# Kernel optimization log

Hardware: AMD Instinct MI355X
Metric: run time of the kernel (lower is better)

The kernel has to match this reference:

```python
import jax, jax.numpy as jnp
import numpy as np
from jax import lax

EPS = 1e-4


def setup_inputs() -> dict:
    key = jax.random.key(0)
    k1, k2, k3, k4, k5 = jax.random.split(key, 5)
    B, F, P, C = 8192, 512, 64, 100
    return {
        "x": jax.random.normal(k1, (B, F), dtype=jnp.float32),
        "w": jax.random.normal(k2, (P, F), dtype=jnp.float32),
        "xi": jax.random.normal(k3, (1, P), dtype=jnp.float32),
        "eta": jax.random.normal(k4, (1, P), dtype=jnp.float32),
        "beta": jax.random.normal(k5, (P, C), dtype=jnp.float32),
    }


def reference(x, w, xi, eta, beta):
    # Distance layer: squared Euclidean distance to each prototype -> [B, P]
    # ||w_p - x||^2 expressed as GEMM form (same math, efficient)
    d = (jnp.sum(x * x, axis=-1, keepdims=True)
         - 2.0 * (x @ w.T)
         + jnp.sum(w * w, axis=-1))  # [B, P]

    # Distance activation: si = sigmoid(xi) * exp(-eta^2 * d), scaled by per-sample max
    gamma = eta * eta                       # [1, P]
    alpha = jax.nn.sigmoid(xi)              # [1, P]
    si = jnp.exp(-gamma * d) * alpha        # [B, P]
    si = si / (jnp.max(si, axis=-1, keepdims=True) + EPS)

    # Belief masses: u_p normalized beta^2 rows -> mass [B, P, C]
    beta_sq = beta * beta
    u = beta_sq / jnp.sum(beta_sq, axis=-1, keepdims=True)  # [P, C]
    mass = si[..., None] * u[None]                           # [B, P, C]

    # Omega: append residual uncertainty channel -> [B, P, C+1]
    omega = 1.0 - jnp.sum(mass, axis=-1, keepdims=True)
    mass_omega = jnp.concatenate([mass, omega], axis=-1)

    # Sequential Dempster combination over prototypes
    masses = jnp.moveaxis(mass_omega, 1, 0)  # [P, B, C+1]

    def step(m1, m2):
        omega1 = m1[..., -1:]
        omega2 = m2[..., -1:]
        c = m1 * m2 + m1 * omega2 + omega1 * m2
        c = c / (jnp.sum(c, axis=-1, keepdims=True) + EPS)
        return c, None

    m_final, _ = lax.scan(step, masses[0], masses[1:])  # [B, C+1]

    # Final normalization
    return m_final / jnp.sum(m_final, axis=-1, keepdims=True)
```

## Files before the change

kernel.cpp:

```cpp
#include <hip/hip_runtime.h>
#include <math.h>

#define NB 8192
#define NF 512
#define NP 64
#define NC 100
#define NR 16
#define EPSF 1e-4f
#define LOG2E  1.44269504088896340736f

using short8  = __attribute__((ext_vector_type(8))) short;
using floatx4 = __attribute__((ext_vector_type(4))) float;

__device__ __forceinline__ unsigned pk2(float a, float b) {
  return (__float_as_uint(b) & 0xffff0000u) | (__float_as_uint(a) >> 16);
}
__device__ __forceinline__ uint2 pkbf(float4 v) {
  uint2 r; r.x = pk2(v.x, v.y); r.y = pk2(v.z, v.w); return r;
}

#define OFF_XH    0
#define OFF_WH    4352
#define OFF_U     0
#define OFF_SI    21760
#define OFF_PK4   25856
#define OFF_REDB  34048
#define OFF_RMAX  35072
#define OFF_UMAX  35328
#define OFF_XSQL  35584
#define OFF_WSQL  35648
#define OFF_KGAM  35904
#define OFF_ALPH  36160
#define OFF_OMF   36416
#define SMEM_SZ   36448

__global__ __launch_bounds__(256, 2)
void ds_one(const float* __restrict__ x, const float* __restrict__ w,
            const float* __restrict__ xi, const float* __restrict__ eta,
            const float* __restrict__ beta, float* __restrict__ out)
{
  __shared__ __align__(16) char smem[SMEM_SZ];
  short*          xh    = (short*)(smem + OFF_XH);
  short*          wh    = (short*)(smem + OFF_WH);
  unsigned short* u_l   = (unsigned short*)(smem + OFF_U);
  float*          si_l  = (float*)(smem + OFF_SI);
  float4*         pk4   = (float4*)(smem + OFF_PK4);
  float*          redb  = (float*)(smem + OFF_REDB);
  float*          rmax  = (float*)(smem + OFF_RMAX);
  float*          umaxl = (float*)(smem + OFF_UMAX);
  float*          xsql  = (float*)(smem + OFF_XSQL);
  float*          wsql  = (float*)(smem + OFF_WSQL);
  float*          kgaml = (float*)(smem + OFF_KGAM);
  float*          alphl = (float*)(smem + OFF_ALPH);
  float*          omf   = (float*)(smem + OFF_OMF);

  const int t    = threadIdx.x;
  const int R0   = blockIdx.x * NR;
  const int wv   = t >> 6;
  const int wl   = t & 63;
  const int ml   = wl & 15;
  const int qd   = wl >> 4;
  const int pcol = wv * 16 + ml;
  const int xrow = t >> 4, xq = t & 15;

  float xsq_acc = 0.f;
  float wacc[4] = {0.f, 0.f, 0.f, 0.f};
  floatx4 acc = {0.f, 0.f, 0.f, 0.f};
  float4 xr0, xr1, wr[4][2];

  {
    const float* xp = &x[(size_t)(R0 + xrow) * NF + xq * 8];
    xr0 = *(const float4*)&xp[0];  xr1 = *(const float4*)&xp[4];
    #pragma unroll
    for (int g = 0; g < 4; ++g) {
      const int row = wv * 16 + g * 4 + (wl >> 4);
      const float* wp = &w[(size_t)row * NF + xq * 8];
      wr[g][0] = *(const float4*)&wp[0];  wr[g][1] = *(const float4*)&wp[4];
    }
  }
  for (int ch = 0; ch < 4; ++ch) {
    __syncthreads();
    {
      xsq_acc += xr0.x*xr0.x + xr0.y*xr0.y + xr0.z*xr0.z + xr0.w*xr0.w
               + xr1.x*xr1.x + xr1.y*xr1.y + xr1.z*xr1.z + xr1.w*xr1.w;
      *(uint2*)&xh[xrow * 136 + xq * 8]     = pkbf(xr0);
      *(uint2*)&xh[xrow * 136 + xq * 8 + 4] = pkbf(xr1);
    }
    #pragma unroll
    for (int g = 0; g < 4; ++g) {
      const int row = wv * 16 + g * 4 + (wl >> 4);
      float4 a = wr[g][0], b = wr[g][1];
      wacc[g] += a.x*a.x + a.y*a.y + a.z*a.z + a.w*a.w
               + b.x*b.x + b.y*b.y + b.z*b.z + b.w*b.w;
      *(uint2*)&wh[row * 136 + xq * 8]     = pkbf(a);
      *(uint2*)&wh[row * 136 + xq * 8 + 4] = pkbf(b);
    }
    __syncthreads();
    if (ch < 3) {
      const int kb = (ch + 1) * 128;
      const float* xp = &x[(size_t)(R0 + xrow) * NF + kb + xq * 8];
      xr0 = *(const float4*)&xp[0];  xr1 = *(const float4*)&xp[4];
      #pragma unroll
      for (int g = 0; g < 4; ++g) {
        const int row = wv * 16 + g * 4 + (wl >> 4);
        const float* wp = &w[(size_t)row * NF + kb + xq * 8];
        wr[g][0] = *(const float4*)&wp[0];  wr[g][1] = *(const float4*)&wp[4];
      }
    }
    #pragma unroll
    for (int ks = 0; ks < 4; ++ks) {
      short8 a = *(const short8*)&xh[ml * 136 + ks * 32 + qd * 8];
      short8 b = *(const short8*)&wh[(wv * 16 + ml) * 136 + ks * 32 + qd * 8];
      acc = __builtin_amdgcn_mfma_f32_16x16x32_bf16(a, b, acc, 0, 0, 0);
    }
  }

  const int p4 = t >> 2, q4 = t & 3;
  {
    const float* br = beta + p4 * NC + q4 * 25;
    float s = 0.f;
    #pragma unroll 5
    for (int j = 0; j < 25; ++j) { float b = br[j]; s = fmaf(b, b, s); }
    redb[q4 * 64 + p4] = s;
  }
  {
    float s = xsq_acc;
    s += __shfl_xor(s, 1, 64); s += __shfl_xor(s, 2, 64);
    s += __shfl_xor(s, 4, 64); s += __shfl_xor(s, 8, 64);
    if (xq == 0) xsql[xrow] = s;
  }
  #pragma unroll
  for (int g = 0; g < 4; ++g) {
    float s = wacc[g];
    s += __shfl_xor(s, 1, 64); s += __shfl_xor(s, 2, 64);
    s += __shfl_xor(s, 4, 64); s += __shfl_xor(s, 8, 64);
    if (xq == 0) wsql[wv * 16 + g * 4 + (wl >> 4)] = s;
  }
  if (t < 64) {
    float e = eta[t];
    kgaml[t] = -LOG2E * e * e;
    alphl[t] = 1.f / (1.f + __expf(-xi[t]));
  }
  __syncthreads();

  float si4[4];
  {
    const float wq = wsql[pcol], kg = kgaml[pcol], al = alphl[pcol];
    #pragma unroll
    for (int i = 0; i < 4; ++i) {
      float d = xsql[qd * 4 + i] + wq - 2.f * acc[i];
      si4[i] = al * exp2f(kg * d);
    }
    #pragma unroll
    for (int i = 0; i < 4; ++i) {
      float m = si4[i];
      m = fmaxf(m, __shfl_xor(m, 1, 64)); m = fmaxf(m, __shfl_xor(m, 2, 64));
      m = fmaxf(m, __shfl_xor(m, 4, 64)); m = fmaxf(m, __shfl_xor(m, 8, 64));
      if (ml == 0) rmax[(qd * 4 + i) * 4 + wv] = m;
    }
  }
  __syncthreads();

  #pragma unroll
  for (int i = 0; i < 4; ++i) {
    const int row = qd * 4 + i;
    float m = fmaxf(fmaxf(rmax[row * 4 + 0], rmax[row * 4 + 1]),
                    fmaxf(rmax[row * 4 + 2], rmax[row * 4 + 3]));
    si_l[row * 64 + pcol] = si4[i] * (1.f / (m + EPSF));
  }
  {
    const float bi = 1.f / (((redb[p4] + redb[64 + p4]) + redb[128 + p4]) + redb[192 + p4]);
    float um = 0.f;
    #pragma unroll
    for (int i2 = 0; i2 < 8; ++i2) {
      const int q = q4 + 4 * i2;
      float4 uv = make_float4(0.f, 0.f, 0.f, 0.f);
      if (q < 25) {
        const float* br = beta + p4 * NC + q * 4;
        uv.x = br[0]*br[0]*bi; uv.y = br[1]*br[1]*bi;
        uv.z = br[2]*br[2]*bi; uv.w = br[3]*br[3]*bi;
      }
      um = fmaxf(um, fmaxf(fmaxf(uv.x, uv.y), fmaxf(uv.z, uv.w)));
      *(uint2*)&u_l[p4 * 128 + q * 4] = pkbf(uv);
    }
    um = fmaxf(um, __shfl_xor(um, 1, 64));
    um = fmaxf(um, __shfl_xor(um, 2, 64));
    if (q4 == 0) umaxl[p4] = um;
  }
  __syncthreads();

  const int lane = t & 31;
  const int row8 = t >> 5;
  #pragma unroll 1
  for (int pass = 0; pass < 2; ++pass) {
    const int srow = pass * 8 + row8;
    {
      float sp0 = si_l[srow * 64 + lane];
      float sp1 = si_l[srow * 64 + 32 + lane];
      float um0 = umaxl[lane], um1 = umaxl[32 + lane];
      float om0 = 1.f - sp0, om1 = 1.f - sp1;
      float c0 = 1.f / fmaf(sp0, um0, om0);
      float c1 = 1.f / fmaf(sp1, um1, om1);
      float st0 = sp0 * c0, ot0 = om0 * c0;
      float st1 = sp1 * c1, ot1 = om1 * c1;
      float pA = 3.f * ot0, pB = 3.f * ot1;
      #pragma unroll
      for (int d2 = 1; d2 < 32; d2 <<= 1) {
        float uA = __shfl_up(pA, d2, 32);
        float uB = __shfl_up(pB, d2, 32);
        if (lane >= d2) { pA *= uA; pB *= uB; }
      }
      float totA = __shfl(pA, 31, 32);
      float w0 = (lane == 0) ? 0.f : pA * (1.f / 9.f);
      float w1 = (totA * pB) * (1.f / 9.f);
      pk4[row8 * 64 + lane]      = make_float4(st0, ot0, w0, 0.f);
      pk4[row8 * 64 + 32 + lane] = make_float4(st1, ot1, w1, 0.f);
      if (lane == 31) omf[row8] = (totA * pB) * (1.f / 3.f);
    }
    float4 T = make_float4(1.f, 1.f, 1.f, 1.f);
    float4 S = make_float4(0.f, 0.f, 0.f, 0.f);
    for (int p = 63; p >= 0; --p) {
      float4 f  = pk4[row8 * 64 + p];
      uint2 ud  = *(const uint2*)&u_l[p * 128 + lane * 4];
      float u0 = __uint_as_float(ud.x << 16);
      float u1 = __uint_as_float(ud.x & 0xffff0000u);
      float u2 = __uint_as_float(ud.y << 16);
      float u3 = __uint_as_float(ud.y & 0xffff0000u);
      S.x = fmaf(f.z, T.x, S.x); S.y = fmaf(f.z, T.y, S.y);
      S.z = fmaf(f.z, T.z, S.z); S.w = fmaf(f.z, T.w, S.w);
      T.x *= fmaf(f.x, u0, f.y);
      T.y *= fmaf(f.x, u1, f.y);
      T.z *= fmaf(f.x, u2, f.y);
      T.w *= fmaf(f.x, u3, f.y);
    }
    float om = omf[row8];
    float m0 = fmaf(2.f, S.x, T.x) - om;
    float m1 = fmaf(2.f, S.y, T.y) - om;
    float m2 = fmaf(2.f, S.z, T.z) - om;
    float m3 = fmaf(2.f, S.w, T.w) - om;
    if (lane >= 25) { m0 = 0.f; m1 = 0.f; m2 = 0.f; m3 = 0.f; }
    float ss = (m0 + m1) + (m2 + m3);
    #pragma unroll
    for (int msk = 1; msk < 32; msk <<= 1) ss += __shfl_xor(ss, msk, 32);
    float rn = 1.f / (ss + om);
    float* orow = &out[(size_t)(R0 + srow) * 101];
    if (lane < 25) {
      orow[lane * 4 + 0] = m0 * rn; orow[lane * 4 + 1] = m1 * rn;
      orow[lane * 4 + 2] = m2 * rn; orow[lane * 4 + 3] = m3 * rn;
    } else if (lane == 25) {
      orow[100] = om * rn;
    }
  }
}

extern "C" void kernel_launch(void* const* d_in, const int* in_sizes, int n_in,
                              void* d_out, int out_size, void* d_ws, size_t ws_size,
                              hipStream_t stream)
{
  const float* x    = (const float*)d_in[0];
  const float* w    = (const float*)d_in[1];
  const float* xi   = (const float*)d_in[2];
  const float* eta  = (const float*)d_in[3];
  const float* beta = (const float*)d_in[4];
  (void)d_ws; (void)ws_size;
  hipLaunchKernelGGL(ds_one, dim3(NB / NR), dim3(256), 0, stream,
                     x, w, xi, eta, beta, (float*)d_out);
}
```

Baseline: 84.54 us.

## Split Dempster prototype chain across wave halves with register-cached masses

Result: no change. 84.50 us (-0.1%).

```diff
diff --git a/kernel.cpp b/kernel.cpp
--- a/kernel.cpp
+++ b/kernel.cpp
@@ -18,21 +18,23 @@
 __device__ __forceinline__ uint2 pkbf(float4 v) {
   uint2 r; r.x = pk2(v.x, v.y); r.y = pk2(v.z, v.w); return r;
 }
+__device__ __forceinline__ float rlane(float v, int l) {
+  return __uint_as_float(__builtin_amdgcn_readlane(__float_as_uint(v), l));
+}
 
 #define OFF_XH    0
 #define OFF_WH    4352
 #define OFF_U     0
 #define OFF_SI    21760
 #define OFF_PK4   25856
-#define OFF_REDB  34048
-#define OFF_RMAX  35072
-#define OFF_UMAX  35328
-#define OFF_XSQL  35584
-#define OFF_WSQL  35648
-#define OFF_KGAM  35904
-#define OFF_ALPH  36160
-#define OFF_OMF   36416
-#define SMEM_SZ   36448
+#define OFF_REDB  29952
+#define OFF_RMAX  30976
+#define OFF_UMAX  31232
+#define OFF_XSQL  31488
+#define OFF_WSQL  31552
+#define OFF_KGAM  31808
+#define OFF_ALPH  32064
+#define SMEM_SZ   32320
 
 __global__ __launch_bounds__(256, 2)
 void ds_one(const float* __restrict__ x, const float* __restrict__ w,
@@ -52,7 +54,6 @@
   float*          wsql  = (float*)(smem + OFF_WSQL);
   float*          kgaml = (float*)(smem + OFF_KGAM);
   float*          alphl = (float*)(smem + OFF_ALPH);
-  float*          omf   = (float*)(smem + OFF_OMF);
 
   const int t    = threadIdx.x;
   const int R0   = blockIdx.x * NR;
@@ -189,39 +190,40 @@
   }
   __syncthreads();
 
-  const int lane = t & 31;
-  const int row8 = t >> 5;
+  const int l31   = wl & 31;
+  const int cbase = l31 * 4;
+  const int pbase = (wl >> 5) * 32;
+  const bool isA  = (wl < 32);
+
+  uint2 ureg[32];
+  #pragma unroll
+  for (int i = 0; i < 32; ++i)
+    ureg[i] = *(const uint2*)&u_l[(pbase + i) * 128 + cbase];
+
   #pragma unroll 1
-  for (int pass = 0; pass < 2; ++pass) {
-    const int srow = pass * 8 + row8;
-    {
-      float sp0 = si_l[srow * 64 + lane];
-      float sp1 = si_l[srow * 64 + 32 + lane];
-      float um0 = umaxl[lane], um1 = umaxl[32 + lane];
-      float om0 = 1.f - sp0, om1 = 1.f - sp1;
-      float c0 = 1.f / fmaf(sp0, um0, om0);
-      float c1 = 1.f / fmaf(sp1, um1, om1);
-      float st0 = sp0 * c0, ot0 = om0 * c0;
-      float st1 = sp1 * c1, ot1 = om1 * c1;
-      float pA = 3.f * ot0, pB = 3.f * ot1;
-      #pragma unroll
-      for (int d2 = 1; d2 < 32; d2 <<= 1) {
-        float uA = __shfl_up(pA, d2, 32);
-        float uB = __shfl_up(pB, d2, 32);
-        if (lane >= d2) { pA *= uA; pB *= uB; }
-      }
-      float totA = __shfl(pA, 31, 32);
-      float w0 = (lane == 0) ? 0.f : pA * (1.f / 9.f);
-      float w1 = (totA * pB) * (1.f / 9.f);
-      pk4[row8 * 64 + lane]      = make_float4(st0, ot0, w0, 0.f);
-      pk4[row8 * 64 + 32 + lane] = make_float4(st1, ot1, w1, 0.f);
-      if (lane == 31) omf[row8] = (totA * pB) * (1.f / 3.f);
-    }
+  for (int r = 0; r < 4; ++r) {
+    const int srow = wv * 4 + r;
+    float sp = si_l[srow * 64 + wl];
+    float um = umaxl[wl];
+    float om = 1.f - sp;
+    float cn = 1.f / fmaf(sp, um, om);
+    float ST = sp * cn, OT = om * cn;
+    float P3 = 3.f * OT;
+    #pragma unroll
+    for (int d2 = 1; d2 < 64; d2 <<= 1) {
+      float up = __shfl_up(P3, d2, 64);
+      if (wl >= d2) P3 *= up;
+    }
+    float W    = (wl == 0) ? 0.f : P3 * (1.f / 9.f);
+    float omfr = rlane(P3, 63) * (1.f / 3.f);
+    pk4[(wv << 6) + wl] = make_float4(ST, OT, W, 0.f);
+
     float4 T = make_float4(1.f, 1.f, 1.f, 1.f);
     float4 S = make_float4(0.f, 0.f, 0.f, 0.f);
-    for (int p = 63; p >= 0; --p) {
-      float4 f  = pk4[row8 * 64 + p];
-      uint2 ud  = *(const uint2*)&u_l[p * 128 + lane * 4];
+    #pragma unroll
+    for (int i = 31; i >= 0; --i) {
+      float4 f = pk4[(wv << 6) + pbase + i];
+      uint2 ud = ureg[i];
       float u0 = __uint_as_float(ud.x << 16);
       float u1 = __uint_as_float(ud.x & 0xffff0000u);
       float u2 = __uint_as_float(ud.y << 16);
@@ -233,22 +235,34 @@
       T.z *= fmaf(f.x, u2, f.y);
       T.w *= fmaf(f.x, u3, f.y);
     }
-    float om = omf[row8];
-    float m0 = fmaf(2.f, S.x, T.x) - om;
-    float m1 = fmaf(2.f, S.y, T.y) - om;
-    float m2 = fmaf(2.f, S.z, T.z) - om;
-    float m3 = fmaf(2.f, S.w, T.w) - om;
-    if (lane >= 25) { m0 = 0.f; m1 = 0.f; m2 = 0.f; m3 = 0.f; }
+    float4 To, So;
+    To.x = __shfl_xor(T.x, 32, 64); To.y = __shfl_xor(T.y, 32, 64);
+    To.z = __shfl_xor(T.z, 32, 64); To.w = __shfl_xor(T.w, 32, 64);
+    So.x = __shfl_xor(S.x, 32, 64); So.y = __shfl_xor(S.y, 32, 64);
+    So.z = __shfl_xor(S.z, 32, 64); So.w = __shfl_xor(S.w, 32, 64);
+    #define CMB(c) { \
+      float SA = isA ? S.c : So.c; \
+      float TB = isA ? To.c : T.c; \
+      float SB = isA ? So.c : S.c; \
+      S.c = fmaf(SA, TB, SB);  T.c = T.c * To.c; }
+    CMB(x) CMB(y) CMB(z) CMB(w)
+    #undef CMB
+
+    float m0 = fmaf(2.f, S.x, T.x) - omfr;
+    float m1 = fmaf(2.f, S.y, T.y) - omfr;
+    float m2 = fmaf(2.f, S.z, T.z) - omfr;
+    float m3 = fmaf(2.f, S.w, T.w) - omfr;
+    if (l31 >= 25) { m0 = 0.f; m1 = 0.f; m2 = 0.f; m3 = 0.f; }
     float ss = (m0 + m1) + (m2 + m3);
     #pragma unroll
-    for (int msk = 1; msk < 32; msk <<= 1) ss += __shfl_xor(ss, msk, 32);
-    float rn = 1.f / (ss + om);
+    for (int msk = 1; msk < 32; msk <<= 1) ss += __shfl_xor(ss, msk, 64);
+    float rn = 1.f / (ss + omfr);
     float* orow = &out[(size_t)(R0 + srow) * 101];
-    if (lane < 25) {
-      orow[lane * 4 + 0] = m0 * rn; orow[lane * 4 + 1] = m1 * rn;
-      orow[lane * 4 + 2] = m2 * rn; orow[lane * 4 + 3] = m3 * rn;
-    } else if (lane == 25) {
-      orow[100] = om * rn;
+    if (wl < 25) {
+      orow[wl * 4 + 0] = m0 * rn; orow[wl * 4 + 1] = m1 * rn;
+      orow[wl * 4 + 2] = m2 * rn; orow[wl * 4 + 3] = m3 * rn;
+    } else if (wl == 25) {
+      orow[100] = omfr * rn;
     }
   }
 }
```
